# Optimization experiments

Hardware: AMD Instinct MI355X
Metric: run time of the kernel (lower is better)

Reference implementation:

```python
import jax, jax.numpy as jnp
import numpy as np

B, S, D, H = 4, 2048, 1024, 16
Dh = D // H
MAX_WAVELENGTH = 10000.0


def apply_rope(x, positions, head_dim):
    # x: [B, S, H, Dh], positions: [B, S]
    fraction = 2.0 * jnp.arange(head_dim // 2, dtype=jnp.float32) / head_dim
    timescale = MAX_WAVELENGTH ** fraction                     # [Dh/2]
    sinusoid = positions[..., None].astype(jnp.float32) / timescale  # [B, S, Dh/2]
    sinusoid = sinusoid[..., None, :]                          # [B, S, 1, Dh/2]
    sin, cos = jnp.sin(sinusoid), jnp.cos(sinusoid)
    first, second = jnp.split(x, 2, axis=-1)
    out = jnp.concatenate([first * cos - second * sin,
                           second * cos + first * sin], axis=-1)
    return out.astype(x.dtype)


def setup_inputs() -> dict:
    key = jax.random.key(0)
    k0, k1, k2, k3, k4 = jax.random.split(key, 5)
    inputs = jax.random.normal(k0, (B, S, D), dtype=jnp.float32)
    segment_positions = jnp.broadcast_to(jnp.arange(S, dtype=jnp.int32), (B, S))
    # causal mask, broadcastable over heads: [B, 1, S, S]
    mask = jnp.broadcast_to(jnp.tril(jnp.ones((S, S), dtype=bool))[None, None], (B, 1, S, S))
    std = 0.02
    w_q = jax.random.normal(k1, (D, H, Dh), dtype=jnp.float32) * std
    w_k = jax.random.normal(k2, (D, H, Dh), dtype=jnp.float32) * std
    w_v = jax.random.normal(k3, (D, H, Dh), dtype=jnp.float32) * std
    w_out = jax.random.normal(k4, (H, Dh, D), dtype=jnp.float32) * std
    return {"inputs": inputs, "w_q": w_q, "w_k": w_k, "w_v": w_v,
            "w_out": w_out, "segment_positions": segment_positions, "mask": mask}


def reference(inputs, w_q, w_k, w_v, w_out, segment_positions, mask):
    # QKV projections: [B, S, D] x [D, H, Dh] -> [B, S, H, Dh]
    q = jnp.einsum('bsd,dhk->bshk', inputs, w_q)
    k = jnp.einsum('bsd,dhk->bshk', inputs, w_k)
    v = jnp.einsum('bsd,dhk->bshk', inputs, w_v)
    q = apply_rope(q, segment_positions, Dh)
    k = apply_rope(k, segment_positions, Dh)
    q = q / jnp.sqrt(jnp.asarray(Dh, dtype=q.dtype))
    attn = jnp.einsum('bqhd,bkhd->bhqk', q, k)                 # [B, H, S, S]
    big_neg = jnp.finfo(attn.dtype).min
    attn = jnp.where(mask, attn, big_neg)
    attn = jax.nn.softmax(attn, axis=-1)
    x = jnp.einsum('bhqk,bkhd->bqhd', attn, v)                 # [B, S, H, Dh]
    return jnp.einsum('bqhd,hdm->bqm', x, w_out)               # [B, S, D]
```

## Files before the change

### kernel.cpp

```cpp
#include <hip/hip_runtime.h>
#include <stdint.h>
#include <math.h>

#define S_LEN 2048
#define DMODEL 1024
#define NHEAD 16
#define DHEAD 64
#define BATCH 4
#define MROWS (BATCH * S_LEN)

typedef __attribute__((ext_vector_type(8))) short bf16x8;
typedef __attribute__((ext_vector_type(4))) float f32x4;

#define MFMA16(a, b, c) __builtin_amdgcn_mfma_f32_16x16x32_bf16(a, b, c, 0, 0, 0)

__device__ __forceinline__ unsigned short f2b(float f) {
  union { float f; unsigned u; } v; v.f = f;
  unsigned u = v.u;
  return (unsigned short)((u + 0x7FFFu + ((u >> 16) & 1u)) >> 16);
}
__device__ __forceinline__ unsigned pkrn(float a, float b) {
  unsigned ua = __float_as_uint(a) + 0x8000u;
  unsigned ub = __float_as_uint(b) + 0x8000u;
  return __builtin_amdgcn_perm(ub, ua, 0x07060302);
}

__device__ __forceinline__ void async16(const void* g, void* l) {
  __builtin_amdgcn_global_load_lds((const __attribute__((address_space(1))) void*)g,
                                   (__attribute__((address_space(3))) void*)l,
                                   16, 0, 0);
}

struct PrepArgs {
  const float4* x; unsigned short* xb; int n4; int cvtBlocks;
  const float* s[4]; unsigned short* d[4];
};
__global__ __launch_bounds__(256) void prep_kernel(PrepArgs p) {
  __shared__ float T[64][65];
  const int bid = blockIdx.x;
  const int t = threadIdx.x;
  if (bid < p.cvtBlocks) {
    int i = bid * 256 + t;
    if (i < p.n4) {
      float4 v = p.x[i];
      ushort4 o;
      o.x = f2b(v.x); o.y = f2b(v.y); o.z = f2b(v.z); o.w = f2b(v.w);
      *(ushort4*)(p.xb + 4 * (size_t)i) = o;
    }
    return;
  }
  const int tb = bid - p.cvtBlocks;
  const int z = tb >> 8;
  const int rem = tb & 255;
  const int r0 = (rem >> 4) * 64, c0 = (rem & 15) * 64;
  const float* in = p.s[z];
  unsigned short* out = p.d[z];
  int c = t & 63, rr = t >> 6;
#pragma unroll
  for (int i = 0; i < 16; i++) {
    int r = i * 4 + rr;
    T[r][c] = in[(size_t)(r0 + r) * 1024 + c0 + c];
  }
  __syncthreads();
  int r2 = t & 63, cc = t >> 6;
#pragma unroll
  for (int i = 0; i < 16; i++) {
    int c2 = i * 4 + cc;
    out[(size_t)(c0 + c2) * 1024 + r0 + r2] = f2b(T[r2][c2]);
  }
}

__global__ __launch_bounds__(256) void gemm_qkv(const unsigned short* __restrict__ A,
                                                const unsigned short* __restrict__ Bt,
                                                unsigned short* __restrict__ Qr,
                                                unsigned short* __restrict__ Kr,
                                                unsigned short* __restrict__ Vt,
                                                const int* __restrict__ pos) {
  constexpr int K = 1024;
  __shared__ unsigned short As[128 * 64];
  __shared__ unsigned short Bs[128 * 64];
  const int bm = blockIdx.y * 128, bn = blockIdx.x * 128;
  const int t = threadIdx.x;
  const int wave = t >> 6, lane = t & 63, quad = lane >> 4, l16 = lane & 15;
  const int wm = (wave >> 1) * 64, wn = (wave & 1) * 64;
  f32x4 acc[4][4] = {};
  const int srow = lane >> 3;
  const int gcol = (((lane & 7) ^ srow)) * 8;
  const unsigned short* Ag = A + (size_t)(bm + wave * 32 + srow) * K + gcol;
  const unsigned short* Bg = Bt + (size_t)(bn + wave * 32 + srow) * K + gcol;
  unsigned short* AsW = &As[(wave * 32) * 64];
  unsigned short* BsW = &Bs[(wave * 32) * 64];
  const int rsw = l16 & 7;

  for (int k0 = 0; k0 < K; k0 += 64) {
    __syncthreads();
#pragma unroll
    for (int i = 0; i < 4; i++) {
      async16(Ag + (size_t)(i * 8) * K + k0, AsW + i * 8 * 64);
      async16(Bg + (size_t)(i * 8) * K + k0, BsW + i * 8 * 64);
    }
    __syncthreads();
#pragma unroll
    for (int kk = 0; kk < 2; kk++) {
      const int sl = ((kk * 4 + quad) ^ rsw) << 3;
      bf16x8 af[4], bfr[4];
#pragma unroll
      for (int mt = 0; mt < 4; mt++)
        af[mt] = *(const bf16x8*)&As[(wm + mt * 16 + l16) * 64 + sl];
#pragma unroll
      for (int nt = 0; nt < 4; nt++)
        bfr[nt] = *(const bf16x8*)&Bs[(wn + nt * 16 + l16) * 64 + sl];
#pragma unroll
      for (int mt = 0; mt < 4; mt++)
#pragma unroll
        for (int nt = 0; nt < 4; nt++)
          acc[mt][nt] = MFMA16(af[mt], bfr[nt], acc[mt][nt]);
    }
  }

  const int cb = bn + wn;
  if (cb >= 2048) {
    const int h = (cb - 2048) >> 6;
#pragma unroll
    for (int mt = 0; mt < 4; mt++)
#pragma unroll
      for (int nt = 0; nt < 4; nt++) {
        int row = bm + wm + mt * 16 + quad * 4;
        int b = row >> 11, s = row & (S_LEN - 1);
        int dh = nt * 16 + l16;
        ushort4 w4;
        w4.x = f2b(acc[mt][nt][0]); w4.y = f2b(acc[mt][nt][1]);
        w4.z = f2b(acc[mt][nt][2]); w4.w = f2b(acc[mt][nt][3]);
        *(ushort4*)&Vt[((size_t)(b * NHEAD + h) * DHEAD + dh) * S_LEN + s] = w4;
      }
  } else {
    const bool isQ = cb < 1024;
    unsigned short* dst0 = isQ ? Qr : Kr;
    const float scl = isQ ? 0.18033688011112042f : 1.0f;
    const int h = (cb >> 6) & 15;
    const float LT = 0.28782313662425572f;
    float it0 = __expf(-(float)l16 * LT);
    float it1 = __expf(-(float)(16 + l16) * LT);
#pragma unroll
    for (int mt = 0; mt < 4; mt++) {
#pragma unroll
      for (int r = 0; r < 4; r++) {
        int row = bm + wm + mt * 16 + quad * 4 + r;
        int b = row >> 11, s = row & (S_LEN - 1);
        float p = (float)pos[row];
        float a0 = p * it0, a1 = p * it1;
        float sn0 = __sinf(a0), cs0 = __cosf(a0);
        float sn1 = __sinf(a1), cs1 = __cosf(a1);
        float x0 = acc[mt][0][r], x1 = acc[mt][1][r];
        float x2 = acc[mt][2][r], x3 = acc[mt][3][r];
        float o0 = (x0 * cs0 - x2 * sn0) * scl;
        float o2 = (x2 * cs0 + x0 * sn0) * scl;
        float o1 = (x1 * cs1 - x3 * sn1) * scl;
        float o3 = (x3 * cs1 + x1 * sn1) * scl;
        unsigned short* dst =
            dst0 + ((size_t)(b * NHEAD + h) * S_LEN + s) * DHEAD;
        dst[0 * 16 + l16] = f2b(o0);
        dst[1 * 16 + l16] = f2b(o1);
        dst[2 * 16 + l16] = f2b(o2);
        dst[3 * 16 + l16] = f2b(o3);
      }
    }
  }
}

__global__ __launch_bounds__(256) void gemm_out(const unsigned short* __restrict__ A,
                                                const unsigned short* __restrict__ Bt,
                                                float* __restrict__ C) {
  constexpr int K = 1024, N = 1024;
  __shared__ unsigned short As[128 * 64];
  __shared__ unsigned short Bs[128 * 64];
  const int bm = blockIdx.y * 128, bn = blockIdx.x * 128;
  const int t = threadIdx.x;
  const int wave = t >> 6, lane = t & 63, quad = lane >> 4, l16 = lane & 15;
  const int wm = (wave >> 1) * 64, wn = (wave & 1) * 64;
  f32x4 acc[4][4] = {};
  const int srow = lane >> 3;
  const int gcol = (((lane & 7) ^ srow)) * 8;
  const unsigned short* Ag = A + (size_t)(bm + wave * 32 + srow) * K + gcol;
  const unsigned short* Bg = Bt + (size_t)(bn + wave * 32 + srow) * K + gcol;
  unsigned short* AsW = &As[(wave * 32) * 64];
  unsigned short* BsW = &Bs[(wave * 32) * 64];
  const int rsw = l16 & 7;

  for (int k0 = 0; k0 < K; k0 += 64) {
    __syncthreads();
#pragma unroll
    for (int i = 0; i < 4; i++) {
      async16(Ag + (size_t)(i * 8) * K + k0, AsW + i * 8 * 64);
      async16(Bg + (size_t)(i * 8) * K + k0, BsW + i * 8 * 64);
    }
    __syncthreads();
#pragma unroll
    for (int kk = 0; kk < 2; kk++) {
      const int sl = ((kk * 4 + quad) ^ rsw) << 3;
      bf16x8 af[4], bfr[4];
#pragma unroll
      for (int mt = 0; mt < 4; mt++)
        af[mt] = *(const bf16x8*)&As[(wm + mt * 16 + l16) * 64 + sl];
#pragma unroll
      for (int nt = 0; nt < 4; nt++)
        bfr[nt] = *(const bf16x8*)&Bs[(wn + nt * 16 + l16) * 64 + sl];
#pragma unroll
      for (int mt = 0; mt < 4; mt++)
#pragma unroll
        for (int nt = 0; nt < 4; nt++)
          acc[mt][nt] = MFMA16(af[mt], bfr[nt], acc[mt][nt]);
    }
  }
#pragma unroll
  for (int mt = 0; mt < 4; mt++)
#pragma unroll
    for (int nt = 0; nt < 4; nt++)
#pragma unroll
      for (int r = 0; r < 4; r++) {
        int row = bm + wm + mt * 16 + quad * 4 + r;
        int col = bn + wn + nt * 16 + l16;
        C[(size_t)row * N + col] = acc[mt][nt][r];
      }
}

__global__ __launch_bounds__(256, 3) void flash_kernel(const unsigned short* __restrict__ Qr,
                                                       const unsigned short* __restrict__ Kr,
                                                       const unsigned short* __restrict__ Vt,
                                                       unsigned short* __restrict__ Xat) {
  const int idx = blockIdx.x;
  const int j = idx >> 6;
  const int bh = idx & 63;
  const int jB = 31 - j;
  const unsigned short* Qh = Qr + (size_t)bh * S_LEN * DHEAD;
  const unsigned short* Kh = Kr + (size_t)bh * S_LEN * DHEAD;
  const unsigned short* Vh = Vt + (size_t)bh * DHEAD * S_LEN;
  __shared__ unsigned short Ks[2][64 * 64];
  __shared__ unsigned short Vs[2][64 * 64];
  __shared__ unsigned short Pt[4][16 * 64];
  const int t = threadIdx.x, wave = t >> 6, lane = t & 63;
  const int quad = lane >> 4, l16 = lane & 15;
  const int srow = lane >> 3;
  const int gcol = (((lane & 7) ^ srow)) * 8;
  const int rsw = l16 & 7;
  const int qrA = j * 64 + wave * 16 + l16;
  const int qrB = jB * 64 + wave * 16 + l16;

  bf16x8 qfA0 = *(const bf16x8*)(Qh + (size_t)qrA * DHEAD + quad * 8);
  bf16x8 qfA1 = *(const bf16x8*)(Qh + (size_t)qrA * DHEAD + 32 + quad * 8);
  bf16x8 qfB0 = *(const bf16x8*)(Qh + (size_t)qrB * DHEAD + quad * 8);
  bf16x8 qfB1 = *(const bf16x8*)(Qh + (size_t)qrB * DHEAD + 32 + quad * 8);

  f32x4 oA[4] = {}, oB[4] = {};
  float lA = 0.f, lB = 0.f;
  unsigned short* PtW = &Pt[wave][0];
  const int c0 = (quad ^ rsw) << 3;
  const int c1 = ((4 + quad) ^ rsw) << 3;
  const int q1b = quad >> 1, qlo4 = (quad & 1) * 4;
  const int pr = l16 * 64;

  auto stage = [&](int kt, int buf) {
    const int k0 = kt * 64;
#pragma unroll
    for (int i = 0; i < 2; i++) {
      async16(Kh + (size_t)(k0 + wave * 16 + i * 8 + srow) * DHEAD + gcol,
              &Ks[buf][(wave * 16 + i * 8) * 64]);
      async16(Vh + (size_t)(wave * 16 + i * 8 + srow) * S_LEN + k0 + gcol,
              &Vs[buf][(wave * 16 + i * 8) * 64]);
    }
  };

  auto softpv = [&](const unsigned short* V_, f32x4* sc, f32x4* o, float& l,
                    int qr_, bool diag, int k0) {
#pragma unroll
    for (int nt = 0; nt < 4; nt++) {
      float p0, p1, p2, p3;
      if (diag) {
        int kg = k0 + nt * 16 + quad * 4;
        p0 = (kg + 0 > qr_) ? 0.f : exp2f(sc[nt][0]);
        p1 = (kg + 1 > qr_) ? 0.f : exp2f(sc[nt][1]);
        p2 = (kg + 2 > qr_) ? 0.f : exp2f(sc[nt][2]);
        p3 = (kg + 3 > qr_) ? 0.f : exp2f(sc[nt][3]);
      } else {
        p0 = exp2f(sc[nt][0]);
        p1 = exp2f(sc[nt][1]);
        p2 = exp2f(sc[nt][2]);
        p3 = exp2f(sc[nt][3]);
      }
      l += (p0 + p1) + (p2 + p3);
      uint2 w; w.x = pkrn(p0, p1); w.y = pkrn(p2, p3);
      const int slot = ((nt * 2 + q1b) ^ rsw) << 3;
      *(uint2*)&PtW[pr + slot + qlo4] = w;
    }
#pragma unroll
    for (int kk = 0; kk < 2; kk++) {
      bf16x8 pb = *(const bf16x8*)&PtW[pr + (((kk * 4 + quad) ^ rsw) << 3)];
#pragma unroll
      for (int nt = 0; nt < 4; nt++) {
        bf16x8 vb = *(const bf16x8*)&V_[(nt * 16 + l16) * 64 + (kk == 0 ? c0 : c1)];
        o[nt] = MFMA16(vb, pb, o[nt]);
      }
    }
  };

  auto computeAB = [&](int cur, int k0, bool adiag) {
    const unsigned short* K_ = Ks[cur];
    const unsigned short* V_ = Vs[cur];
    f32x4 scA[4] = {}, scB[4] = {};
#pragma unroll
    for (int nt = 0; nt < 4; nt++) {
      bf16x8 kb0 = *(const bf16x8*)&K_[(nt * 16 + l16) * 64 + c0];
      bf16x8 kb1 = *(const bf16x8*)&K_[(nt * 16 + l16) * 64 + c1];
      scA[nt] = MFMA16(kb0, qfA0, scA[nt]);
      scA[nt] = MFMA16(kb1, qfA1, scA[nt]);
      scB[nt] = MFMA16(kb0, qfB0, scB[nt]);
      scB[nt] = MFMA16(kb1, qfB1, scB[nt]);
    }
    softpv(V_, scA, oA, lA, qrA, adiag, k0);
    softpv(V_, scB, oB, lB, qrB, false, k0);
  };

  auto computeB = [&](int cur, int k0, bool bdiag) {
    const unsigned short* K_ = Ks[cur];
    const unsigned short* V_ = Vs[cur];
    f32x4 scB[4] = {};
#pragma unroll
    for (int nt = 0; nt < 4; nt++) {
      bf16x8 kb0 = *(const bf16x8*)&K_[(nt * 16 + l16) * 64 + c0];
      bf16x8 kb1 = *(const bf16x8*)&K_[(nt * 16 + l16) * 64 + c1];
      scB[nt] = MFMA16(kb0, qfB0, scB[nt]);
      scB[nt] = MFMA16(kb1, qfB1, scB[nt]);
    }
    softpv(V_, scB, oB, lB, qrB, bdiag, k0);
  };

  stage(0, 0);
  int cur = 0;
  for (int kt = 0; kt < j; ++kt) {
    __syncthreads();
    stage(kt + 1, cur ^ 1);
    computeAB(cur, kt * 64, false);
    cur ^= 1;
  }
  __syncthreads();
  stage(j + 1, cur ^ 1);
  computeAB(cur, j * 64, true);
  cur ^= 1;
  for (int kt = j + 1; kt < jB; ++kt) {
    __syncthreads();
    stage(kt + 1, cur ^ 1);
    computeB(cur, kt * 64, false);
    cur ^= 1;
  }
  __syncthreads();
  computeB(cur, jB * 64, true);

  lA += __shfl_xor(lA, 16); lA += __shfl_xor(lA, 32);
  lB += __shfl_xor(lB, 16); lB += __shfl_xor(lB, 32);
  const float ivA = 1.0f / lA, ivB = 1.0f / lB;
  const int b = bh >> 4, h = bh & 15;
  unsigned short* dA = Xat + (size_t)(b * S_LEN + qrA) * DMODEL + h * DHEAD;
  unsigned short* dB = Xat + (size_t)(b * S_LEN + qrB) * DMODEL + h * DHEAD;
#pragma unroll
  for (int nt = 0; nt < 4; nt++) {
    ushort4 wa, wb;
    wa.x = f2b(oA[nt][0] * ivA); wa.y = f2b(oA[nt][1] * ivA);
    wa.z = f2b(oA[nt][2] * ivA); wa.w = f2b(oA[nt][3] * ivA);
    wb.x = f2b(oB[nt][0] * ivB); wb.y = f2b(oB[nt][1] * ivB);
    wb.z = f2b(oB[nt][2] * ivB); wb.w = f2b(oB[nt][3] * ivB);
    *(ushort4*)(dA + nt * 16 + quad * 4) = wa;
    *(ushort4*)(dB + nt * 16 + quad * 4) = wb;
  }
}

extern "C" void kernel_launch(void* const* d_in, const int* in_sizes, int n_in,
                              void* d_out, int out_size, void* d_ws, size_t ws_size,
                              hipStream_t stream) {
  const float* x = (const float*)d_in[0];
  const float* wq = (const float*)d_in[1];
  const float* wk = (const float*)d_in[2];
  const float* wv = (const float*)d_in[3];
  const float* wo = (const float*)d_in[4];
  const int* pos = (const int*)d_in[5];
  float* out = (float*)d_out;
  char* ws = (char*)d_ws;

  const size_t EL_X = (size_t)MROWS * DMODEL;
  const size_t EL_W = (size_t)DMODEL * DMODEL;
  unsigned short* Xb = (unsigned short*)ws;
  unsigned short* Wqkv = Xb + EL_X;
  unsigned short* WoT = Wqkv + 3 * EL_W;
  unsigned short* Qr = WoT + EL_W;
  unsigned short* Kr = Qr + EL_X;
  unsigned short* Vt = Kr + EL_X;
  unsigned short* Xat = Vt + EL_X;

  PrepArgs pa;
  pa.x = (const float4*)x; pa.xb = Xb;
  pa.n4 = (int)(EL_X / 4);
  pa.cvtBlocks = (int)(EL_X / 4 / 256);
  pa.s[0] = wq; pa.d[0] = Wqkv;
  pa.s[1] = wk; pa.d[1] = Wqkv + EL_W;
  pa.s[2] = wv; pa.d[2] = Wqkv + 2 * EL_W;
  pa.s[3] = wo; pa.d[3] = WoT;
  prep_kernel<<<pa.cvtBlocks + 1024, 256, 0, stream>>>(pa);

  dim3 gq(24, 64);
  gemm_qkv<<<gq, 256, 0, stream>>>(Xb, Wqkv, Qr, Kr, Vt, pos);
  flash_kernel<<<1024, 256, 0, stream>>>(Qr, Kr, Vt, Xat);
  dim3 gg(8, 64);
  gemm_out<<<gg, 256, 0, stream>>>(Xat, WoT, out);
}
```

Baseline: 299.0 us.

## Pair adjacent query tiles per block and reorder causal work for balance

Each block now handles two adjacent 64-row query tiles (a 128-row band) instead of pairing tile j with 31-j. The two tiles share every K/V tile except the last, so both compute paths run together through nearly the whole loop. Band indices are permuted across the block index so heavy and light blocks interleave for load balance. The double-buffer loop is unrolled by two with fixed buffer indices. Per-block work is now uneven, so completion depends on how the scheduler places the permuted blocks.

```diff
diff --git a/kernel.cpp b/kernel.cpp
--- a/kernel.cpp
+++ b/kernel.cpp
@@ -230,8 +230,9 @@
                                                        unsigned short* __restrict__ Xat) {
   const int idx = blockIdx.x;
   const int j = idx >> 6;
+  const int c = j & 3, kcl = j >> 2;
+  const int qt = (kcl == 0) ? 15 - c : (kcl == 1) ? 7 - c : (kcl == 2) ? 8 + c : c;
   const int bh = idx & 63;
-  const int jB = 31 - j;
   const unsigned short* Qh = Qr + (size_t)bh * S_LEN * DHEAD;
   const unsigned short* Kh = Kr + (size_t)bh * S_LEN * DHEAD;
   const unsigned short* Vh = Vt + (size_t)bh * DHEAD * S_LEN;
@@ -243,8 +244,9 @@
   const int srow = lane >> 3;
   const int gcol = (((lane & 7) ^ srow)) * 8;
   const int rsw = l16 & 7;
-  const int qrA = j * 64 + wave * 16 + l16;
-  const int qrB = jB * 64 + wave * 16 + l16;
+  const int q0 = qt * 128;
+  const int qrA = q0 + wave * 16 + l16;
+  const int qrB = qrA + 64;
 
   bf16x8 qfA0 = *(const bf16x8*)(Qh + (size_t)qrA * DHEAD + quad * 8);
   bf16x8 qfA1 = *(const bf16x8*)(Qh + (size_t)qrA * DHEAD + 32 + quad * 8);
@@ -320,9 +322,24 @@
     softpv(V_, scB, oB, lB, qrB, false, k0);
   };
 
-  auto computeB = [&](int cur, int k0, bool bdiag) {
-    const unsigned short* K_ = Ks[cur];
-    const unsigned short* V_ = Vs[cur];
+  stage(0, 0);
+  const int kmax = 2 * qt;
+  int kt = 0;
+  for (; kt < kmax; kt += 2) {
+    __syncthreads();
+    stage(kt + 1, 1);
+    computeAB(0, kt * 64, false);
+    __syncthreads();
+    stage(kt + 2, 0);
+    computeAB(1, (kt + 1) * 64, false);
+  }
+  __syncthreads();
+  stage(kmax + 1, 1);
+  computeAB(0, kmax * 64, true);
+  __syncthreads();
+  {
+    const unsigned short* K_ = Ks[1];
+    const unsigned short* V_ = Vs[1];
     f32x4 scB[4] = {};
 #pragma unroll
     for (int nt = 0; nt < 4; nt++) {
@@ -331,29 +348,8 @@
       scB[nt] = MFMA16(kb0, qfB0, scB[nt]);
       scB[nt] = MFMA16(kb1, qfB1, scB[nt]);
     }
-    softpv(V_, scB, oB, lB, qrB, bdiag, k0);
-  };
-
-  stage(0, 0);
-  int cur = 0;
-  for (int kt = 0; kt < j; ++kt) {
-    __syncthreads();
-    stage(kt + 1, cur ^ 1);
-    computeAB(cur, kt * 64, false);
-    cur ^= 1;
-  }
-  __syncthreads();
-  stage(j + 1, cur ^ 1);
-  computeAB(cur, j * 64, true);
-  cur ^= 1;
-  for (int kt = j + 1; kt < jB; ++kt) {
-    __syncthreads();
-    stage(kt + 1, cur ^ 1);
-    computeB(cur, kt * 64, false);
-    cur ^= 1;
-  }
-  __syncthreads();
-  computeB(cur, jB * 64, true);
+    softpv(V_, scB, oB, lB, qrB, true, (kmax + 1) * 64);
+  }
 
   lA += __shfl_xor(lA, 16); lA += __shfl_xor(lA, 32);
   lB += __shfl_xor(lB, 16); lB += __shfl_xor(lB, 32);
```

Measured after the change: 287.4 us. -3.9%, faster.
